# Performance work log

Hardware: AMD Instinct MI355X
Metric: run time of the kernel (lower is better)

The kernel has to match this reference:

```python
import jax, jax.numpy as jnp
import numpy as np

N_NODES = 100000
N_EDGES = 1600000
N_GRAPHS = 128
BEHAVIOR_DIM = 32
LLM_DIM = 768
LLM_PROJ = 32
HIDDEN = 64
NUM_CLASSES = 2
INPUT_DIM = 64 + 16 + LLM_PROJ + BEHAVIOR_DIM  # 144


def gcn_conv(h, edge_index, edge_weight, W, b, n):
    """PyG GCNConv: linear -> gcn_norm with self-loops -> scatter-add at target."""
    h = h @ W  # [N, out]
    row, col = edge_index[0], edge_index[1]
    loop = jnp.arange(n)
    row_f = jnp.concatenate([row, loop])
    col_f = jnp.concatenate([col, loop])
    ew_f = jnp.concatenate([edge_weight, jnp.ones((n,), h.dtype)])
    deg = jax.ops.segment_sum(ew_f, col_f, num_segments=n)
    dinv = jnp.where(deg > 0, jax.lax.rsqrt(deg), 0.0)
    norm = dinv[row_f] * ew_f * dinv[col_f]  # [E+N]
    out = jax.ops.segment_sum(norm[:, None] * h[row_f], col_f, num_segments=n)
    return out + b


def global_mean_pool(x, batch, num_graphs):
    s = jax.ops.segment_sum(x, batch, num_segments=num_graphs)
    cnt = jax.ops.segment_sum(jnp.ones((x.shape[0],), x.dtype), batch, num_segments=num_graphs)
    return s / jnp.maximum(cnt, 1.0)[:, None]


def setup_inputs() -> dict:
    key = jax.random.key(0)
    ks = jax.random.split(key, 16)
    inp = {
        "x_names": jax.random.randint(ks[0], (N_NODES,), 0, 20000),
        "x_types": jax.random.randint(ks[1], (N_NODES,), 0, 100),
        "x_behaviors": jax.random.normal(ks[2], (N_NODES, BEHAVIOR_DIM), jnp.float32),
        "edge_index": jax.random.randint(ks[3], (2, N_EDGES), 0, N_NODES),
        "edge_weight": jax.random.uniform(ks[4], (N_EDGES,), jnp.float32),
        "batch": jnp.sort(jax.random.randint(ks[5], (N_NODES,), 0, N_GRAPHS)),
        "llm_features": jax.random.normal(ks[6], (N_NODES, LLM_DIM), jnp.float32),
        # parameters
        "name_emb": jax.random.normal(ks[7], (20000, 64), jnp.float32),
        "type_emb": jax.random.normal(ks[8], (100, 16), jnp.float32),
        "llm_proj_w": jax.random.normal(ks[9], (LLM_DIM, LLM_PROJ), jnp.float32) * 0.02,
        "llm_proj_b": jnp.zeros((LLM_PROJ,), jnp.float32),
        "conv1_w": jax.random.normal(ks[10], (INPUT_DIM, HIDDEN), jnp.float32) * 0.08,
        "conv1_b": jnp.zeros((HIDDEN,), jnp.float32),
        "conv2_w": jax.random.normal(ks[11], (HIDDEN, HIDDEN), jnp.float32) * 0.12,
        "conv2_b": jnp.zeros((HIDDEN,), jnp.float32),
        "cls_w": jax.random.normal(ks[12], (HIDDEN, NUM_CLASSES), jnp.float32) * 0.12,
        "cls_b": jnp.zeros((NUM_CLASSES,), jnp.float32),
    }
    return inp


def reference(x_names, x_types, x_behaviors, edge_index, edge_weight, batch,
              llm_features, name_emb, type_emb, llm_proj_w, llm_proj_b,
              conv1_w, conv1_b, conv2_w, conv2_b, cls_w, cls_b):
    n = x_names.shape[0]
    name_feat = name_emb[x_names]          # [N, 64]
    type_feat = type_emb[x_types]          # [N, 16]
    llm_feat = llm_features @ llm_proj_w + llm_proj_b  # [N, 32]
    x = jnp.concatenate([name_feat, type_feat, llm_feat, x_behaviors], axis=1)
    # dropout is identity in eval mode
    x = jax.nn.relu(gcn_conv(x, edge_index, edge_weight, conv1_w, conv1_b, n))
    x = jax.nn.relu(gcn_conv(x, edge_index, edge_weight, conv2_w, conv2_b, n))
    x = global_mean_pool(x, batch, N_GRAPHS)  # [G, HIDDEN]
    return x @ cls_w + cls_b                   # [G, 2]
```

## Files before the change

### kernel.cpp

```cpp
#include <hip/hip_runtime.h>
#include <cstdint>
#include <cstddef>

typedef __attribute__((ext_vector_type(8))) _Float16 f16x8;
typedef __attribute__((ext_vector_type(4))) _Float16 f16x4;
typedef __attribute__((ext_vector_type(4))) float f32x4;

__device__ __forceinline__ f16x8 cvt8(const float4& p, const float4& q) {
  f16x8 r;
  r[0] = (_Float16)p.x; r[1] = (_Float16)p.y; r[2] = (_Float16)p.z; r[3] = (_Float16)p.w;
  r[4] = (_Float16)q.x; r[5] = (_Float16)q.y; r[6] = (_Float16)q.z; r[7] = (_Float16)q.w;
  return r;
}


__global__ void prep_kernel(const float* __restrict__ pw, const float* __restrict__ pb,
                            const float* __restrict__ w1, const float* __restrict__ w2,
                            _Float16* __restrict__ Bf, float* __restrict__ biasf,
                            _Float16* __restrict__ B2f) {
  int idx = blockIdx.x * 256 + threadIdx.x;
  if (idx < 896 * 64) {
    int gk = idx >> 6, col = idx & 63;
    float val;
    if (gk < 768) {
      float acc = 0.0f;
      #pragma unroll 8
      for (int m = 0; m < 32; ++m) acc = fmaf(pw[gk * 32 + m], w1[(80 + m) * 64 + col], acc);
      val = acc;
    } else if (gk < 832) val = w1[(gk - 768) * 64 + col];
    else if (gk < 848)   val = w1[(64 + gk - 832) * 64 + col];
    else if (gk < 864)   val = w1[(112 + gk - 848) * 64 + col];
    else if (gk < 880)   val = w1[(128 + gk - 864) * 64 + col];
    else                 val = 0.0f;
    int chunk = gk >> 5, k = gk & 31;
    int g, j;
    if (k < 16) { g = k >> 2; j = k & 3; } else { int k2 = k - 16; g = k2 >> 2; j = 4 + (k2 & 3); }
    Bf[((size_t)(chunk * 4 + g) * 64 + col) * 8 + j] = (_Float16)val;
  } else if (idx < 896 * 64 + 64) {
    int col = idx - 896 * 64;
    float acc = 0.0f;
    for (int m = 0; m < 32; ++m) acc = fmaf(pb[m], w1[(80 + m) * 64 + col], acc);
    biasf[col] = acc;
  } else if (idx < 896 * 64 + 64 + 64 * 64) {
    int q2 = idx - (896 * 64 + 64);
    int gk = q2 >> 6, col = q2 & 63;
    float val = w2[gk * 64 + col];
    int chunk = gk >> 5, k = gk & 31;
    int g, j;
    if (k < 16) { g = k >> 2; j = k & 3; } else { int k2 = k - 16; g = k2 >> 2; j = 4 + (k2 & 3); }
    B2f[((size_t)(chunk * 4 + g) * 64 + col) * 8 + j] = (_Float16)val;
  }
}


__global__ void cnt_kernel(const int* __restrict__ ei, int* __restrict__ cnt, int E) {
  int e = blockIdx.x * 256 + threadIdx.x;
  if (e < E) atomicAdd(&cnt[ei[E + e]], 1);
}

__global__ __launch_bounds__(256) void scan_blk(const int* __restrict__ cnt,
                                                int* __restrict__ colp,
                                                int* __restrict__ bsum, int n) {
  __shared__ int ws[4];
  int t = threadIdx.x, lane = t & 63, w = t >> 6;
  int i = blockIdx.x * 256 + t;
  int v = (i < n) ? cnt[i] : 0;
  int x = v;
  #pragma unroll
  for (int off = 1; off < 64; off <<= 1) { int y = __shfl_up(x, off); if (lane >= off) x += y; }
  if (lane == 63) ws[w] = x;
  __syncthreads();
  if (t == 0) {
    int s = 0;
    #pragma unroll
    for (int k = 0; k < 4; ++k) { int tmp = ws[k]; ws[k] = s; s += tmp; }
    bsum[blockIdx.x] = s;
  }
  __syncthreads();
  if (i < n) colp[i] = ws[w] + x - v;
}

__global__ __launch_bounds__(512) void scan_top(int* __restrict__ bsum,
                                                int* __restrict__ colp, int nb, int n) {
  __shared__ int ws[8];
  int t = threadIdx.x, lane = t & 63, w = t >> 6;
  int v = (t < nb) ? bsum[t] : 0;
  int x = v;
  #pragma unroll
  for (int off = 1; off < 64; off <<= 1) { int y = __shfl_up(x, off); if (lane >= off) x += y; }
  if (lane == 63) ws[w] = x;
  __syncthreads();
  if (t == 0) {
    int s = 0;
    #pragma unroll
    for (int k = 0; k < 8; ++k) { int tmp = ws[k]; ws[k] = s; s += tmp; }
  }
  __syncthreads();
  int excl = ws[w] + x - v;
  if (t < nb) bsum[t] = excl;
  if (t == nb - 1) colp[n] = excl + v;
}

__global__ void scan_add(int* __restrict__ colp, int* __restrict__ fillp,
                         const int* __restrict__ bsum, int n) {
  int i = blockIdx.x * 256 + threadIdx.x;
  if (i < n) {
    int c = colp[i] + bsum[blockIdx.x];
    colp[i] = c;
    fillp[i] = c;
  }
}

__global__ void fill_kernel(const int* __restrict__ ei, const float* __restrict__ ew,
                            int* __restrict__ fillp, int2* __restrict__ csr, int E) {
  int e = blockIdx.x * 256 + threadIdx.x;
  if (e >= E) return;
  int row = ei[e], col = ei[E + e];
  int pos = atomicAdd(&fillp[col], 1);
  csr[pos] = make_int2(row, __float_as_int(ew[e]));
}

__global__ void degsum_kernel(const int* __restrict__ colp, const int2* __restrict__ csr,
                              float* __restrict__ dinv, int n) {
  int j = blockIdx.x * 256 + threadIdx.x;
  if (j >= n) return;
  int e0 = colp[j], e1 = colp[j + 1];
  float s = 1.0f;
  for (int e = e0; e < e1; ++e) s += __int_as_float(csr[e].y);
  dinv[j] = rsqrtf(s);
}


__device__ __forceinline__ void loadBf(const _Float16* __restrict__ Bf, int c, int g, int r16,
                                       f16x8 (&bf)[4]) {
  #pragma unroll
  for (int ct = 0; ct < 4; ++ct)
    bf[ct] = *(const f16x8*)(Bf + ((size_t)(c * 4 + g) * 64 + ct * 16 + r16) * 8);
}

__device__ __forceinline__ void mfma8(f32x4 (&acc)[2][4], const f16x8& a0, const f16x8& a1,
                                      const f16x8 (&bf)[4]) {
  #pragma unroll
  for (int ct = 0; ct < 4; ++ct) {
    acc[0][ct] = __builtin_amdgcn_mfma_f32_16x16x32_f16(a0, bf[ct], acc[0][ct], 0, 0, 0);
    acc[1][ct] = __builtin_amdgcn_mfma_f32_16x16x32_f16(a1, bf[ct], acc[1][ct], 0, 0, 0);
  }
}

__global__ __launch_bounds__(256, 3) void gemm1_kernel(
    const float* __restrict__ llm, const _Float16* __restrict__ Bf,
    const int* __restrict__ names, const int* __restrict__ types,
    const float* __restrict__ beh, const float* __restrict__ nemb,
    const float* __restrict__ temb, const float* __restrict__ biasf,
    const float* __restrict__ dinv, _Float16* __restrict__ out, int n)
{
  int nwg = gridDim.x;
  int b = blockIdx.x;
  int q = nwg >> 3, r = nwg & 7;
  int xcd = b & 7, bidx = b >> 3;
  int swz = (xcd < r ? xcd * (q + 1) : r * (q + 1) + (xcd - r) * q) + bidx;

  int w = swz * 4 + (threadIdx.x >> 6);
  int nw = (n + 31) >> 5;
  if (w >= nw) return;
  int lane = threadIdx.x & 63;
  int g = lane >> 4, r16 = lane & 15;
  int base = w * 32;

  int arow0 = base + r16;      if (arow0 > n - 1) arow0 = n - 1;
  int arow1 = base + 16 + r16; if (arow1 > n - 1) arow1 = n - 1;
  int nm0 = names[arow0], nm1 = names[arow1];
  int tp0 = types[arow0], tp1 = types[arow1];

  const float* pA0 = llm + (size_t)arow0 * 768 + g * 4;
  const float* pA1 = llm + (size_t)arow1 * 768 + g * 4;

  f32x4 acc[2][4];
  #pragma unroll
  for (int i = 0; i < 2; ++i)
    #pragma unroll
    for (int j = 0; j < 4; ++j) { acc[i][j][0] = 0.f; acc[i][j][1] = 0.f; acc[i][j][2] = 0.f; acc[i][j][3] = 0.f; }

  float4 X0l = *(const float4*)(pA0 +  0), X0h = *(const float4*)(pA0 + 16);
  float4 X1l = *(const float4*)(pA1 +  0), X1h = *(const float4*)(pA1 + 16);
  float4 Y0l = *(const float4*)(pA0 + 32), Y0h = *(const float4*)(pA0 + 48);
  float4 Y1l = *(const float4*)(pA1 + 32), Y1h = *(const float4*)(pA1 + 48);
  float4 Z0l = *(const float4*)(pA0 + 64), Z0h = *(const float4*)(pA0 + 80);
  float4 Z1l = *(const float4*)(pA1 + 64), Z1h = *(const float4*)(pA1 + 80);

  f16x8 bf[4], a0, a1;

  #pragma unroll 1
  for (int cc = 0; cc < 7; ++cc) {
    const int c = cc * 3;
    loadBf(Bf, c, g, r16, bf);
    a0 = cvt8(X0l, X0h); a1 = cvt8(X1l, X1h);
    X0l = *(const float4*)(pA0 + (c + 3) * 32);
    X0h = *(const float4*)(pA0 + (c + 3) * 32 + 16);
    X1l = *(const float4*)(pA1 + (c + 3) * 32);
    X1h = *(const float4*)(pA1 + (c + 3) * 32 + 16);
    __builtin_amdgcn_sched_barrier(0);
    mfma8(acc, a0, a1, bf);
    loadBf(Bf, c + 1, g, r16, bf);
    a0 = cvt8(Y0l, Y0h); a1 = cvt8(Y1l, Y1h);
    Y0l = *(const float4*)(pA0 + (c + 4) * 32);
    Y0h = *(const float4*)(pA0 + (c + 4) * 32 + 16);
    Y1l = *(const float4*)(pA1 + (c + 4) * 32);
    Y1h = *(const float4*)(pA1 + (c + 4) * 32 + 16);
    __builtin_amdgcn_sched_barrier(0);
    mfma8(acc, a0, a1, bf);
    loadBf(Bf, c + 2, g, r16, bf);
    a0 = cvt8(Z0l, Z0h); a1 = cvt8(Z1l, Z1h);
    Z0l = *(const float4*)(pA0 + (c + 5) * 32);
    Z0h = *(const float4*)(pA0 + (c + 5) * 32 + 16);
    Z1l = *(const float4*)(pA1 + (c + 5) * 32);
    Z1h = *(const float4*)(pA1 + (c + 5) * 32 + 16);
    __builtin_amdgcn_sched_barrier(0);
    mfma8(acc, a0, a1, bf);
  }

  loadBf(Bf, 21, g, r16, bf);
  a0 = cvt8(X0l, X0h); a1 = cvt8(X1l, X1h);
  mfma8(acc, a0, a1, bf);
  loadBf(Bf, 22, g, r16, bf);
  a0 = cvt8(Y0l, Y0h); a1 = cvt8(Y1l, Y1h);
  mfma8(acc, a0, a1, bf);
  loadBf(Bf, 23, g, r16, bf);
  a0 = cvt8(Z0l, Z0h); a1 = cvt8(Z1l, Z1h);
  mfma8(acc, a0, a1, bf);

  const float* pN0 = nemb + (size_t)nm0 * 64 + g * 4;
  const float* pN1 = nemb + (size_t)nm1 * 64 + g * 4;
  #pragma unroll
  for (int t = 0; t < 2; ++t) {
    float4 l0 = *(const float4*)(pN0 + t * 32), h0 = *(const float4*)(pN0 + t * 32 + 16);
    float4 l1 = *(const float4*)(pN1 + t * 32), h1 = *(const float4*)(pN1 + t * 32 + 16);
    loadBf(Bf, 24 + t, g, r16, bf);
    a0 = cvt8(l0, h0); a1 = cvt8(l1, h1);
    mfma8(acc, a0, a1, bf);
  }
  {
    float4 l0 = *(const float4*)(temb + (size_t)tp0 * 16 + g * 4);
    float4 h0 = *(const float4*)(beh + (size_t)arow0 * 32 + g * 4);
    float4 l1 = *(const float4*)(temb + (size_t)tp1 * 16 + g * 4);
    float4 h1 = *(const float4*)(beh + (size_t)arow1 * 32 + g * 4);
    loadBf(Bf, 26, g, r16, bf);
    a0 = cvt8(l0, h0); a1 = cvt8(l1, h1);
    mfma8(acc, a0, a1, bf);
  }
  {
    const float4 z = make_float4(0.f, 0.f, 0.f, 0.f);
    float4 l0 = *(const float4*)(beh + (size_t)arow0 * 32 + 16 + g * 4);
    float4 l1 = *(const float4*)(beh + (size_t)arow1 * 32 + 16 + g * 4);
    loadBf(Bf, 27, g, r16, bf);
    a0 = cvt8(l0, z); a1 = cvt8(l1, z);
    mfma8(acc, a0, a1, bf);
  }

  float dv0[4], dv1[4];
  #pragma unroll
  for (int rr = 0; rr < 4; ++rr) {
    int n0 = base + g * 4 + rr;      dv0[rr] = dinv[n0 < n ? n0 : n - 1];
    int n1 = base + 16 + g * 4 + rr; dv1[rr] = dinv[n1 < n ? n1 : n - 1];
  }
  #pragma unroll
  for (int ct = 0; ct < 4; ++ct) {
    int col = ct * 16 + r16;
    float bfc = biasf[col];
    #pragma unroll
    for (int rr = 0; rr < 4; ++rr) {
      int node0 = base + g * 4 + rr;
      if (node0 < n) out[(size_t)node0 * 64 + col] = (_Float16)((acc[0][ct][rr] + bfc) * dv0[rr]);
      int node1 = base + 16 + g * 4 + rr;
      if (node1 < n) out[(size_t)node1 * 64 + col] = (_Float16)((acc[1][ct][rr] + bfc) * dv1[rr]);
    }
  }
}


__global__ __launch_bounds__(256, 4) void gemm2_kernel(
    const _Float16* __restrict__ h, const _Float16* __restrict__ B2f,
    const float* __restrict__ dinv, _Float16* __restrict__ out, int n)
{
  int w = blockIdx.x * 4 + (threadIdx.x >> 6);
  int nw = (n + 31) >> 5;
  if (w >= nw) return;
  int lane = threadIdx.x & 63;
  int g = lane >> 4, r16 = lane & 15;
  int base = w * 32;
  int arow0 = base + r16;      if (arow0 > n - 1) arow0 = n - 1;
  int arow1 = base + 16 + r16; if (arow1 > n - 1) arow1 = n - 1;

  f32x4 acc[2][4];
  #pragma unroll
  for (int i = 0; i < 2; ++i)
    #pragma unroll
    for (int j = 0; j < 4; ++j) { acc[i][j][0] = 0.f; acc[i][j][1] = 0.f; acc[i][j][2] = 0.f; acc[i][j][3] = 0.f; }

  #pragma unroll
  for (int c = 0; c < 2; ++c) {
    f16x8 bf[4];
    loadBf(B2f, c, g, r16, bf);
    const _Float16* p0 = h + (size_t)arow0 * 64 + c * 32 + g * 4;
    const _Float16* p1 = h + (size_t)arow1 * 64 + c * 32 + g * 4;
    f16x4 lo0 = *(const f16x4*)p0, hi0 = *(const f16x4*)(p0 + 16);
    f16x4 lo1 = *(const f16x4*)p1, hi1 = *(const f16x4*)(p1 + 16);
    f16x8 a0, a1;
    a0[0] = lo0[0]; a0[1] = lo0[1]; a0[2] = lo0[2]; a0[3] = lo0[3];
    a0[4] = hi0[0]; a0[5] = hi0[1]; a0[6] = hi0[2]; a0[7] = hi0[3];
    a1[0] = lo1[0]; a1[1] = lo1[1]; a1[2] = lo1[2]; a1[3] = lo1[3];
    a1[4] = hi1[0]; a1[5] = hi1[1]; a1[6] = hi1[2]; a1[7] = hi1[3];
    mfma8(acc, a0, a1, bf);
  }

  float dv0[4], dv1[4];
  #pragma unroll
  for (int rr = 0; rr < 4; ++rr) {
    int n0 = base + g * 4 + rr;      dv0[rr] = dinv[n0 < n ? n0 : n - 1];
    int n1 = base + 16 + g * 4 + rr; dv1[rr] = dinv[n1 < n ? n1 : n - 1];
  }
  #pragma unroll
  for (int ct = 0; ct < 4; ++ct) {
    int col = ct * 16 + r16;
    #pragma unroll
    for (int rr = 0; rr < 4; ++rr) {
      int node0 = base + g * 4 + rr;
      if (node0 < n) out[(size_t)node0 * 64 + col] = (_Float16)(acc[0][ct][rr] * dv0[rr]);
      int node1 = base + 16 + g * 4 + rr;
      if (node1 < n) out[(size_t)node1 * 64 + col] = (_Float16)(acc[1][ct][rr] * dv1[rr]);
    }
  }
}


template <typename OUT>
__global__ __launch_bounds__(256) void agg_kernel(
    const _Float16* __restrict__ hp, const int* __restrict__ colp,
    const int2* __restrict__ csr, const float* __restrict__ dinv,
    const float* __restrict__ bias, OUT* __restrict__ out, int n)
{
  int wid = threadIdx.x >> 6, lane = threadIdx.x & 63;
  int j = blockIdx.x * 4 + wid;
  if (j >= n) return;
  float dj = dinv[j];
  float hj = (float)hp[(size_t)j * 64 + lane];
  int e0 = colp[j], e1 = colp[j + 1];
  float s0 = 0.0f, s1 = 0.0f;
  int e = e0;
  for (; e + 8 <= e1; e += 8) {
    int2 m0 = csr[e],     m1 = csr[e + 1], m2 = csr[e + 2], m3 = csr[e + 3];
    int2 m4 = csr[e + 4], m5 = csr[e + 5], m6 = csr[e + 6], m7 = csr[e + 7];
    float f0 = (float)hp[(size_t)m0.x * 64 + lane];
    float f1 = (float)hp[(size_t)m1.x * 64 + lane];
    float f2 = (float)hp[(size_t)m2.x * 64 + lane];
    float f3 = (float)hp[(size_t)m3.x * 64 + lane];
    float f4 = (float)hp[(size_t)m4.x * 64 + lane];
    float f5 = (float)hp[(size_t)m5.x * 64 + lane];
    float f6 = (float)hp[(size_t)m6.x * 64 + lane];
    float f7 = (float)hp[(size_t)m7.x * 64 + lane];
    s0 = fmaf(__int_as_float(m0.y), f0, s0);
    s1 = fmaf(__int_as_float(m1.y), f1, s1);
    s0 = fmaf(__int_as_float(m2.y), f2, s0);
    s1 = fmaf(__int_as_float(m3.y), f3, s1);
    s0 = fmaf(__int_as_float(m4.y), f4, s0);
    s1 = fmaf(__int_as_float(m5.y), f5, s1);
    s0 = fmaf(__int_as_float(m6.y), f6, s0);
    s1 = fmaf(__int_as_float(m7.y), f7, s1);
  }
  for (; e + 2 <= e1; e += 2) {
    int2 m0 = csr[e], m1 = csr[e + 1];
    float f0 = (float)hp[(size_t)m0.x * 64 + lane];
    float f1 = (float)hp[(size_t)m1.x * 64 + lane];
    s0 = fmaf(__int_as_float(m0.y), f0, s0);
    s1 = fmaf(__int_as_float(m1.y), f1, s1);
  }
  if (e < e1) {
    int2 m = csr[e];
    s0 = fmaf(__int_as_float(m.y), (float)hp[(size_t)m.x * 64 + lane], s0);
  }
  float acc = bias[lane] + dj * (hj + s0 + s1);
  out[(size_t)j * 64 + lane] = (OUT)fmaxf(acc, 0.0f);
}


__global__ __launch_bounds__(256) void pool_kernel(const float* __restrict__ x,
                                                   const int* __restrict__ batch,
                                                   float* __restrict__ pooled, int n) {
  __shared__ float red[4][64];
  __shared__ int range_s[2];
  int gph = blockIdx.x;
  int tid = threadIdx.x, wid = tid >> 6, lane = tid & 63;
  if (tid < 2) {
    int target = gph + tid;
    int lo = 0, hi = n;
    while (lo < hi) { int m = (lo + hi) >> 1; if (batch[m] < target) lo = m + 1; else hi = m; }
    range_s[tid] = lo;
  }
  __syncthreads();
  int lo = range_s[0], hi = range_s[1];
  float acc = 0.0f;
  for (int i = lo + wid; i < hi; i += 4) acc += x[(size_t)i * 64 + lane];
  red[wid][lane] = acc;
  __syncthreads();
  if (tid < 64) {
    float sum = red[0][lane] + red[1][lane] + red[2][lane] + red[3][lane];
    float cntf = (float)(hi - lo);
    pooled[gph * 64 + lane] = sum / fmaxf(cntf, 1.0f);
  }
}

__global__ void cls_kernel(const float* __restrict__ pooled, const float* __restrict__ cw,
                           const float* __restrict__ cb, float* __restrict__ out) {
  int t = threadIdx.x;
  int gph = t >> 1, c = t & 1;
  float acc = cb[c];
  #pragma unroll 8
  for (int k = 0; k < 64; ++k) acc = fmaf(pooled[gph * 64 + k], cw[k * 2 + c], acc);
  out[gph * 2 + c] = acc;
}


extern "C" void kernel_launch(void* const* d_in, const int* in_sizes, int n_in,
                              void* d_out, int out_size, void* d_ws, size_t ws_size,
                              hipStream_t stream) {
  const int*   x_names  = (const int*)  d_in[0];
  const int*   x_types  = (const int*)  d_in[1];
  const float* behav    = (const float*)d_in[2];
  const int*   ei       = (const int*)  d_in[3];
  const float* ew       = (const float*)d_in[4];
  const int*   batch    = (const int*)  d_in[5];
  const float* llm      = (const float*)d_in[6];
  const float* name_emb = (const float*)d_in[7];
  const float* type_emb = (const float*)d_in[8];
  const float* pw       = (const float*)d_in[9];
  const float* pb       = (const float*)d_in[10];
  const float* w1       = (const float*)d_in[11];
  const float* b1       = (const float*)d_in[12];
  const float* w2       = (const float*)d_in[13];
  const float* b2       = (const float*)d_in[14];
  const float* cw       = (const float*)d_in[15];
  const float* cb       = (const float*)d_in[16];

  const int N = in_sizes[0];
  const int E = in_sizes[4];
  const int nb = (N + 255) / 256;
  const int eb = (E + 255) / 256;
  const int gblocks = ((N + 31) / 32 + 3) / 4;

  char* p = (char*)d_ws;
  auto alloc = [&](size_t bytes) -> void* {
    void* r = (void*)p; p += (bytes + 255) & ~(size_t)255; return r;
  };
  float*     dinv   = (float*)    alloc((size_t)N * 4);
  int*       cnt    = (int*)      alloc((size_t)N * 4);
  int*       colp   = (int*)      alloc((size_t)(N + 1) * 4);
  int*       fillp  = (int*)      alloc((size_t)N * 4);
  int2*      csr    = (int2*)     alloc((size_t)E * 8);
  int*       bsum   = (int*)      alloc((size_t)(nb + 1) * 4);
  _Float16*  Bf     = (_Float16*) alloc((size_t)896 * 64 * 2);
  _Float16*  B2f    = (_Float16*) alloc((size_t)64 * 64 * 2);
  float*     biasf  = (float*)    alloc((size_t)64 * 4);
  _Float16*  hp1    = (_Float16*) alloc((size_t)N * 64 * 2);
  _Float16*  y1     = (_Float16*) alloc((size_t)N * 64 * 2);
  _Float16*  hp2    = (_Float16*) alloc((size_t)N * 64 * 2);
  float*     y2     = (float*)    alloc((size_t)N * 64 * 4);
  float*     pooled = (float*)    alloc((size_t)128 * 64 * 4);
  (void)ws_size; (void)n_in; (void)out_size;

  prep_kernel<<<(896 * 64 + 64 + 64 * 64 + 255) / 256, 256, 0, stream>>>(
      pw, pb, w1, w2, Bf, biasf, B2f);
  hipMemsetAsync(cnt, 0, (size_t)N * 4, stream);
  cnt_kernel<<<eb, 256, 0, stream>>>(ei, cnt, E);
  scan_blk<<<nb, 256, 0, stream>>>(cnt, colp, bsum, N);
  scan_top<<<1, 512, 0, stream>>>(bsum, colp, nb, N);
  scan_add<<<nb, 256, 0, stream>>>(colp, fillp, bsum, N);
  fill_kernel<<<eb, 256, 0, stream>>>(ei, ew, fillp, csr, E);
  degsum_kernel<<<nb, 256, 0, stream>>>(colp, csr, dinv, N);

  gemm1_kernel<<<gblocks, 256, 0, stream>>>(llm, Bf, x_names, x_types, behav,
                                            name_emb, type_emb, biasf, dinv, hp1, N);
  agg_kernel<_Float16><<<(N + 3) / 4, 256, 0, stream>>>(hp1, colp, csr, dinv, b1, y1, N);
  gemm2_kernel<<<gblocks, 256, 0, stream>>>(y1, B2f, dinv, hp2, N);
  agg_kernel<float><<<(N + 3) / 4, 256, 0, stream>>>(hp2, colp, csr, dinv, b2, y2, N);
  pool_kernel<<<128, 256, 0, stream>>>(y2, batch, pooled, N);
  cls_kernel<<<1, 256, 0, stream>>>(pooled, cw, cb, (float*)d_out);
}
```

Baseline: 479.8 us.

## Vectorize aggregation gathers, contiguous K-layout for MFMA, fold memset and fillp

The aggregation kernel now splits each wave into four edge groups of 16 lanes, with each lane gathering four contiguous f16 features. Partial sums are combined with cross-lane shuffles, which replaces 64 scalar 2-byte gathers per edge with wider 8-byte loads. The MFMA K-permutation now packs 8 contiguous K elements per lane group, so A operands load as contiguous float4 pairs and gemm2 loads f16x8 directly. The cnt memset is folded into prep_kernel and the separate fillp array is removed by filling CSR with atomics on colp, reading the shifted offsets afterwards.

```diff
diff --git a/kernel.cpp b/kernel.cpp
--- a/kernel.cpp
+++ b/kernel.cpp
@@ -13,12 +13,20 @@
   return r;
 }
 
+__device__ __forceinline__ void store4(_Float16* p, const float4& v) {
+  f16x4 r;
+  r[0] = (_Float16)v.x; r[1] = (_Float16)v.y; r[2] = (_Float16)v.z; r[3] = (_Float16)v.w;
+  *(f16x4*)p = r;
+}
+__device__ __forceinline__ void store4(float* p, const float4& v) { *(float4*)p = v; }
+
 
 __global__ void prep_kernel(const float* __restrict__ pw, const float* __restrict__ pb,
                             const float* __restrict__ w1, const float* __restrict__ w2,
                             _Float16* __restrict__ Bf, float* __restrict__ biasf,
-                            _Float16* __restrict__ B2f) {
+                            _Float16* __restrict__ B2f, int* __restrict__ cnt, int n) {
   int idx = blockIdx.x * 256 + threadIdx.x;
+  if (idx < n) cnt[idx] = 0;
   if (idx < 896 * 64) {
     int gk = idx >> 6, col = idx & 63;
     float val;
@@ -33,8 +41,7 @@
     else if (gk < 880)   val = w1[(128 + gk - 864) * 64 + col];
     else                 val = 0.0f;
     int chunk = gk >> 5, k = gk & 31;
-    int g, j;
-    if (k < 16) { g = k >> 2; j = k & 3; } else { int k2 = k - 16; g = k2 >> 2; j = 4 + (k2 & 3); }
+    int g = k >> 3, j = k & 7;
     Bf[((size_t)(chunk * 4 + g) * 64 + col) * 8 + j] = (_Float16)val;
   } else if (idx < 896 * 64 + 64) {
     int col = idx - 896 * 64;
@@ -46,8 +53,7 @@
     int gk = q2 >> 6, col = q2 & 63;
     float val = w2[gk * 64 + col];
     int chunk = gk >> 5, k = gk & 31;
-    int g, j;
-    if (k < 16) { g = k >> 2; j = k & 3; } else { int k2 = k - 16; g = k2 >> 2; j = 4 + (k2 & 3); }
+    int g = k >> 3, j = k & 7;
     B2f[((size_t)(chunk * 4 + g) * 64 + col) * 8 + j] = (_Float16)val;
   }
 }
@@ -101,22 +107,17 @@
   if (t == nb - 1) colp[n] = excl + v;
 }
 
-__global__ void scan_add(int* __restrict__ colp, int* __restrict__ fillp,
-                         const int* __restrict__ bsum, int n) {
+__global__ void scan_add(int* __restrict__ colp, const int* __restrict__ bsum, int n) {
   int i = blockIdx.x * 256 + threadIdx.x;
-  if (i < n) {
-    int c = colp[i] + bsum[blockIdx.x];
-    colp[i] = c;
-    fillp[i] = c;
-  }
+  if (i < n) colp[i] += bsum[blockIdx.x];
 }
 
 __global__ void fill_kernel(const int* __restrict__ ei, const float* __restrict__ ew,
-                            int* __restrict__ fillp, int2* __restrict__ csr, int E) {
+                            int* __restrict__ colp, int2* __restrict__ csr, int E) {
   int e = blockIdx.x * 256 + threadIdx.x;
   if (e >= E) return;
   int row = ei[e], col = ei[E + e];
-  int pos = atomicAdd(&fillp[col], 1);
+  int pos = atomicAdd(&colp[col], 1);
   csr[pos] = make_int2(row, __float_as_int(ew[e]));
 }
 
@@ -124,7 +125,8 @@
                               float* __restrict__ dinv, int n) {
   int j = blockIdx.x * 256 + threadIdx.x;
   if (j >= n) return;
-  int e0 = colp[j], e1 = colp[j + 1];
+  int e0 = (j > 0) ? colp[j - 1] : 0;
+  int e1 = colp[j];
   float s = 1.0f;
   for (int e = e0; e < e1; ++e) s += __int_as_float(csr[e].y);
   dinv[j] = rsqrtf(s);
@@ -172,8 +174,8 @@
   int nm0 = names[arow0], nm1 = names[arow1];
   int tp0 = types[arow0], tp1 = types[arow1];
 
-  const float* pA0 = llm + (size_t)arow0 * 768 + g * 4;
-  const float* pA1 = llm + (size_t)arow1 * 768 + g * 4;
+  const float* pA0 = llm + (size_t)arow0 * 768 + g * 8;
+  const float* pA1 = llm + (size_t)arow1 * 768 + g * 8;
 
   f32x4 acc[2][4];
   #pragma unroll
@@ -181,12 +183,12 @@
     #pragma unroll
     for (int j = 0; j < 4; ++j) { acc[i][j][0] = 0.f; acc[i][j][1] = 0.f; acc[i][j][2] = 0.f; acc[i][j][3] = 0.f; }
 
-  float4 X0l = *(const float4*)(pA0 +  0), X0h = *(const float4*)(pA0 + 16);
-  float4 X1l = *(const float4*)(pA1 +  0), X1h = *(const float4*)(pA1 + 16);
-  float4 Y0l = *(const float4*)(pA0 + 32), Y0h = *(const float4*)(pA0 + 48);
-  float4 Y1l = *(const float4*)(pA1 + 32), Y1h = *(const float4*)(pA1 + 48);
-  float4 Z0l = *(const float4*)(pA0 + 64), Z0h = *(const float4*)(pA0 + 80);
-  float4 Z1l = *(const float4*)(pA1 + 64), Z1h = *(const float4*)(pA1 + 80);
+  float4 X0l = *(const float4*)(pA0 +  0), X0h = *(const float4*)(pA0 +  4);
+  float4 X1l = *(const float4*)(pA1 +  0), X1h = *(const float4*)(pA1 +  4);
+  float4 Y0l = *(const float4*)(pA0 + 32), Y0h = *(const float4*)(pA0 + 36);
+  float4 Y1l = *(const float4*)(pA1 + 32), Y1h = *(const float4*)(pA1 + 36);
+  float4 Z0l = *(const float4*)(pA0 + 64), Z0h = *(const float4*)(pA0 + 68);
+  float4 Z1l = *(const float4*)(pA1 + 64), Z1h = *(const float4*)(pA1 + 68);
 
   f16x8 bf[4], a0, a1;
 
@@ -196,25 +198,25 @@
     loadBf(Bf, c, g, r16, bf);
     a0 = cvt8(X0l, X0h); a1 = cvt8(X1l, X1h);
     X0l = *(const float4*)(pA0 + (c + 3) * 32);
-    X0h = *(const float4*)(pA0 + (c + 3) * 32 + 16);
+    X0h = *(const float4*)(pA0 + (c + 3) * 32 + 4);
     X1l = *(const float4*)(pA1 + (c + 3) * 32);
-    X1h = *(const float4*)(pA1 + (c + 3) * 32 + 16);
+    X1h = *(const float4*)(pA1 + (c + 3) * 32 + 4);
     __builtin_amdgcn_sched_barrier(0);
     mfma8(acc, a0, a1, bf);
     loadBf(Bf, c + 1, g, r16, bf);
     a0 = cvt8(Y0l, Y0h); a1 = cvt8(Y1l, Y1h);
     Y0l = *(const float4*)(pA0 + (c + 4) * 32);
-    Y0h = *(const float4*)(pA0 + (c + 4) * 32 + 16);
+    Y0h = *(const float4*)(pA0 + (c + 4) * 32 + 4);
     Y1l = *(const float4*)(pA1 + (c + 4) * 32);
-    Y1h = *(const float4*)(pA1 + (c + 4) * 32 + 16);
+    Y1h = *(const float4*)(pA1 + (c + 4) * 32 + 4);
     __builtin_amdgcn_sched_barrier(0);
     mfma8(acc, a0, a1, bf);
     loadBf(Bf, c + 2, g, r16, bf);
     a0 = cvt8(Z0l, Z0h); a1 = cvt8(Z1l, Z1h);
     Z0l = *(const float4*)(pA0 + (c + 5) * 32);
-    Z0h = *(const float4*)(pA0 + (c + 5) * 32 + 16);
+    Z0h = *(const float4*)(pA0 + (c + 5) * 32 + 4);
     Z1l = *(const float4*)(pA1 + (c + 5) * 32);
-    Z1h = *(const float4*)(pA1 + (c + 5) * 32 + 16);
+    Z1h = *(const float4*)(pA1 + (c + 5) * 32 + 4);
     __builtin_amdgcn_sched_barrier(0);
     mfma8(acc, a0, a1, bf);
   }
@@ -229,31 +231,36 @@
   a0 = cvt8(Z0l, Z0h); a1 = cvt8(Z1l, Z1h);
   mfma8(acc, a0, a1, bf);
 
-  const float* pN0 = nemb + (size_t)nm0 * 64 + g * 4;
-  const float* pN1 = nemb + (size_t)nm1 * 64 + g * 4;
+  const float* pN0 = nemb + (size_t)nm0 * 64 + g * 8;
+  const float* pN1 = nemb + (size_t)nm1 * 64 + g * 8;
   #pragma unroll
   for (int t = 0; t < 2; ++t) {
-    float4 l0 = *(const float4*)(pN0 + t * 32), h0 = *(const float4*)(pN0 + t * 32 + 16);
-    float4 l1 = *(const float4*)(pN1 + t * 32), h1 = *(const float4*)(pN1 + t * 32 + 16);
+    float4 l0 = *(const float4*)(pN0 + t * 32), h0 = *(const float4*)(pN0 + t * 32 + 4);
+    float4 l1 = *(const float4*)(pN1 + t * 32), h1 = *(const float4*)(pN1 + t * 32 + 4);
     loadBf(Bf, 24 + t, g, r16, bf);
     a0 = cvt8(l0, h0); a1 = cvt8(l1, h1);
     mfma8(acc, a0, a1, bf);
   }
   {
-    float4 l0 = *(const float4*)(temb + (size_t)tp0 * 16 + g * 4);
-    float4 h0 = *(const float4*)(beh + (size_t)arow0 * 32 + g * 4);
-    float4 l1 = *(const float4*)(temb + (size_t)tp1 * 16 + g * 4);
-    float4 h1 = *(const float4*)(beh + (size_t)arow1 * 32 + g * 4);
+    const float* q0 = (g < 2) ? (temb + (size_t)tp0 * 16 + g * 8)
+                              : (beh + (size_t)arow0 * 32 + (g - 2) * 8);
+    const float* q1 = (g < 2) ? (temb + (size_t)tp1 * 16 + g * 8)
+                              : (beh + (size_t)arow1 * 32 + (g - 2) * 8);
+    float4 l0 = *(const float4*)q0, h0 = *(const float4*)(q0 + 4);
+    float4 l1 = *(const float4*)q1, h1 = *(const float4*)(q1 + 4);
     loadBf(Bf, 26, g, r16, bf);
     a0 = cvt8(l0, h0); a1 = cvt8(l1, h1);
     mfma8(acc, a0, a1, bf);
   }
   {
     const float4 z = make_float4(0.f, 0.f, 0.f, 0.f);
-    float4 l0 = *(const float4*)(beh + (size_t)arow0 * 32 + 16 + g * 4);
-    float4 l1 = *(const float4*)(beh + (size_t)arow1 * 32 + 16 + g * 4);
+    const float* r0 = beh + (size_t)arow0 * 32 + 16 + (g & 1) * 8;
+    const float* r1 = beh + (size_t)arow1 * 32 + 16 + (g & 1) * 8;
+    float4 l0 = *(const float4*)r0, h0 = *(const float4*)(r0 + 4);
+    float4 l1 = *(const float4*)r1, h1 = *(const float4*)(r1 + 4);
+    if (g >= 2) { l0 = z; h0 = z; l1 = z; h1 = z; }
     loadBf(Bf, 27, g, r16, bf);
-    a0 = cvt8(l0, z); a1 = cvt8(l1, z);
+    a0 = cvt8(l0, h0); a1 = cvt8(l1, h1);
     mfma8(acc, a0, a1, bf);
   }
 
@@ -301,15 +308,8 @@
   for (int c = 0; c < 2; ++c) {
     f16x8 bf[4];
     loadBf(B2f, c, g, r16, bf);
-    const _Float16* p0 = h + (size_t)arow0 * 64 + c * 32 + g * 4;
-    const _Float16* p1 = h + (size_t)arow1 * 64 + c * 32 + g * 4;
-    f16x4 lo0 = *(const f16x4*)p0, hi0 = *(const f16x4*)(p0 + 16);
-    f16x4 lo1 = *(const f16x4*)p1, hi1 = *(const f16x4*)(p1 + 16);
-    f16x8 a0, a1;
-    a0[0] = lo0[0]; a0[1] = lo0[1]; a0[2] = lo0[2]; a0[3] = lo0[3];
-    a0[4] = hi0[0]; a0[5] = hi0[1]; a0[6] = hi0[2]; a0[7] = hi0[3];
-    a1[0] = lo1[0]; a1[1] = lo1[1]; a1[2] = lo1[2]; a1[3] = lo1[3];
-    a1[4] = hi1[0]; a1[5] = hi1[1]; a1[6] = hi1[2]; a1[7] = hi1[3];
+    f16x8 a0 = *(const f16x8*)(h + (size_t)arow0 * 64 + c * 32 + g * 8);
+    f16x8 a1 = *(const f16x8*)(h + (size_t)arow1 * 64 + c * 32 + g * 8);
     mfma8(acc, a0, a1, bf);
   }
 
@@ -342,44 +342,54 @@
   int wid = threadIdx.x >> 6, lane = threadIdx.x & 63;
   int j = blockIdx.x * 4 + wid;
   if (j >= n) return;
-  float dj = dinv[j];
-  float hj = (float)hp[(size_t)j * 64 + lane];
-  int e0 = colp[j], e1 = colp[j + 1];
-  float s0 = 0.0f, s1 = 0.0f;
-  int e = e0;
-  for (; e + 8 <= e1; e += 8) {
-    int2 m0 = csr[e],     m1 = csr[e + 1], m2 = csr[e + 2], m3 = csr[e + 3];
-    int2 m4 = csr[e + 4], m5 = csr[e + 5], m6 = csr[e + 6], m7 = csr[e + 7];
-    float f0 = (float)hp[(size_t)m0.x * 64 + lane];
-    float f1 = (float)hp[(size_t)m1.x * 64 + lane];
-    float f2 = (float)hp[(size_t)m2.x * 64 + lane];
-    float f3 = (float)hp[(size_t)m3.x * 64 + lane];
-    float f4 = (float)hp[(size_t)m4.x * 64 + lane];
-    float f5 = (float)hp[(size_t)m5.x * 64 + lane];
-    float f6 = (float)hp[(size_t)m6.x * 64 + lane];
-    float f7 = (float)hp[(size_t)m7.x * 64 + lane];
-    s0 = fmaf(__int_as_float(m0.y), f0, s0);
-    s1 = fmaf(__int_as_float(m1.y), f1, s1);
-    s0 = fmaf(__int_as_float(m2.y), f2, s0);
-    s1 = fmaf(__int_as_float(m3.y), f3, s1);
-    s0 = fmaf(__int_as_float(m4.y), f4, s0);
-    s1 = fmaf(__int_as_float(m5.y), f5, s1);
-    s0 = fmaf(__int_as_float(m6.y), f6, s0);
-    s1 = fmaf(__int_as_float(m7.y), f7, s1);
-  }
-  for (; e + 2 <= e1; e += 2) {
-    int2 m0 = csr[e], m1 = csr[e + 1];
-    float f0 = (float)hp[(size_t)m0.x * 64 + lane];
-    float f1 = (float)hp[(size_t)m1.x * 64 + lane];
-    s0 = fmaf(__int_as_float(m0.y), f0, s0);
-    s1 = fmaf(__int_as_float(m1.y), f1, s1);
-  }
-  if (e < e1) {
+  int gid = lane >> 4, sl = lane & 15;
+  int e0 = (j > 0) ? colp[j - 1] : 0;
+  int e1 = colp[j];
+
+  float4 s0 = make_float4(0.f, 0.f, 0.f, 0.f);
+  float4 s1 = make_float4(0.f, 0.f, 0.f, 0.f);
+  int e = e0 + gid;
+  for (; e + 12 < e1; e += 16) {
+    int2 m0 = csr[e], m1 = csr[e + 4], m2 = csr[e + 8], m3 = csr[e + 12];
+    f16x4 v0 = *(const f16x4*)(hp + (size_t)m0.x * 64 + sl * 4);
+    f16x4 v1 = *(const f16x4*)(hp + (size_t)m1.x * 64 + sl * 4);
+    f16x4 v2 = *(const f16x4*)(hp + (size_t)m2.x * 64 + sl * 4);
+    f16x4 v3 = *(const f16x4*)(hp + (size_t)m3.x * 64 + sl * 4);
+    float w0 = __int_as_float(m0.y), w1 = __int_as_float(m1.y);
+    float w2 = __int_as_float(m2.y), w3 = __int_as_float(m3.y);
+    s0.x = fmaf(w0, (float)v0[0], s0.x); s0.y = fmaf(w0, (float)v0[1], s0.y);
+    s0.z = fmaf(w0, (float)v0[2], s0.z); s0.w = fmaf(w0, (float)v0[3], s0.w);
+    s1.x = fmaf(w1, (float)v1[0], s1.x); s1.y = fmaf(w1, (float)v1[1], s1.y);
+    s1.z = fmaf(w1, (float)v1[2], s1.z); s1.w = fmaf(w1, (float)v1[3], s1.w);
+    s0.x = fmaf(w2, (float)v2[0], s0.x); s0.y = fmaf(w2, (float)v2[1], s0.y);
+    s0.z = fmaf(w2, (float)v2[2], s0.z); s0.w = fmaf(w2, (float)v2[3], s0.w);
+    s1.x = fmaf(w3, (float)v3[0], s1.x); s1.y = fmaf(w3, (float)v3[1], s1.y);
+    s1.z = fmaf(w3, (float)v3[2], s1.z); s1.w = fmaf(w3, (float)v3[3], s1.w);
+  }
+  for (; e < e1; e += 4) {
     int2 m = csr[e];
-    s0 = fmaf(__int_as_float(m.y), (float)hp[(size_t)m.x * 64 + lane], s0);
-  }
-  float acc = bias[lane] + dj * (hj + s0 + s1);
-  out[(size_t)j * 64 + lane] = (OUT)fmaxf(acc, 0.0f);
+    f16x4 v = *(const f16x4*)(hp + (size_t)m.x * 64 + sl * 4);
+    float w0 = __int_as_float(m.y);
+    s0.x = fmaf(w0, (float)v[0], s0.x); s0.y = fmaf(w0, (float)v[1], s0.y);
+    s0.z = fmaf(w0, (float)v[2], s0.z); s0.w = fmaf(w0, (float)v[3], s0.w);
+  }
+  float4 t = make_float4(s0.x + s1.x, s0.y + s1.y, s0.z + s1.z, s0.w + s1.w);
+  t.x += __shfl_xor(t.x, 16); t.y += __shfl_xor(t.y, 16);
+  t.z += __shfl_xor(t.z, 16); t.w += __shfl_xor(t.w, 16);
+  t.x += __shfl_xor(t.x, 32); t.y += __shfl_xor(t.y, 32);
+  t.z += __shfl_xor(t.z, 32); t.w += __shfl_xor(t.w, 32);
+
+  if (gid == 0) {
+    float dj = dinv[j];
+    f16x4 h4 = *(const f16x4*)(hp + (size_t)j * 64 + sl * 4);
+    float4 bb = *(const float4*)(bias + sl * 4);
+    float4 r;
+    r.x = fmaxf(fmaf(dj, (float)h4[0] + t.x, bb.x), 0.f);
+    r.y = fmaxf(fmaf(dj, (float)h4[1] + t.y, bb.y), 0.f);
+    r.z = fmaxf(fmaf(dj, (float)h4[2] + t.z, bb.z), 0.f);
+    r.w = fmaxf(fmaf(dj, (float)h4[3] + t.w, bb.w), 0.f);
+    store4(out + (size_t)j * 64 + sl * 4, r);
+  }
 }
 
 
@@ -454,7 +464,6 @@
   float*     dinv   = (float*)    alloc((size_t)N * 4);
   int*       cnt    = (int*)      alloc((size_t)N * 4);
   int*       colp   = (int*)      alloc((size_t)(N + 1) * 4);
-  int*       fillp  = (int*)      alloc((size_t)N * 4);
   int2*      csr    = (int2*)     alloc((size_t)E * 8);
   int*       bsum   = (int*)      alloc((size_t)(nb + 1) * 4);
   _Float16*  Bf     = (_Float16*) alloc((size_t)896 * 64 * 2);
@@ -467,14 +476,14 @@
   float*     pooled = (float*)    alloc((size_t)128 * 64 * 4);
   (void)ws_size; (void)n_in; (void)out_size;
 
-  prep_kernel<<<(896 * 64 + 64 + 64 * 64 + 255) / 256, 256, 0, stream>>>(
-      pw, pb, w1, w2, Bf, biasf, B2f);
-  hipMemsetAsync(cnt, 0, (size_t)N * 4, stream);
+  int prep_blocks = (896 * 64 + 64 + 64 * 64 + 255) / 256;
+  if (prep_blocks < nb) prep_blocks = nb;
+  prep_kernel<<<prep_blocks, 256, 0, stream>>>(pw, pb, w1, w2, Bf, biasf, B2f, cnt, N);
   cnt_kernel<<<eb, 256, 0, stream>>>(ei, cnt, E);
   scan_blk<<<nb, 256, 0, stream>>>(cnt, colp, bsum, N);
   scan_top<<<1, 512, 0, stream>>>(bsum, colp, nb, N);
-  scan_add<<<nb, 256, 0, stream>>>(colp, fillp, bsum, N);
-  fill_kernel<<<eb, 256, 0, stream>>>(ei, ew, fillp, csr, E);
+  scan_add<<<nb, 256, 0, stream>>>(colp, bsum, N);
+  fill_kernel<<<eb, 256, 0, stream>>>(ei, ew, colp, csr, E);
   degsum_kernel<<<nb, 256, 0, stream>>>(colp, csr, dinv, N);
 
   gemm1_kernel<<<gblocks, 256, 0, stream>>>(llm, Bf, x_names, x_types, behav,
```

After: 496.4 us. +3.5%, slower.
